# Optimization experiments

Measured on AMD Instinct MI355X. Metric: run time of the kernel, lower is better.

The kernel has to match this reference:

```python
import jax, jax.numpy as jnp
import numpy as np

N = 16384            # number of input vectors
CODEBOOK_SIZE = 8192  # M
DIM = 256             # dim_feature
BETA = 0.25           # commitment_weight


def setup_inputs() -> dict:
    key = jax.random.key(0)
    kx, ke = jax.random.split(key)
    x = jax.random.normal(kx, (N, DIM), dtype=jnp.float32)
    # kaiming-uniform-style init for the codebook
    bound = float(np.sqrt(3.0 / DIM))
    embeddings = jax.random.uniform(ke, (CODEBOOK_SIZE, DIM), dtype=jnp.float32,
                                    minval=-bound, maxval=bound)
    return {"x": x, "embeddings": embeddings}


def reference(x, embeddings):
    # l2_dist: sqrt(sum((x_i - e_j)^2)) computed via the GEMM expansion
    x2 = jnp.sum(x * x, axis=1, keepdims=True)               # (N, 1)
    e2 = jnp.sum(embeddings * embeddings, axis=1)            # (M,)
    d2 = x2 + e2[None, :] - 2.0 * (x @ embeddings.T)         # (N, M)
    dist = jnp.sqrt(jnp.maximum(d2, 0.0))
    # deterministic gumbel_sample path (training eval / stochastic=False):
    # argmax of logits = -dist  <=>  argmin of dist
    ind = jnp.argmin(dist, axis=1)                           # (N,)
    quantized = embeddings[ind]                              # one_hot @ embeddings
    # commitment loss: beta * ||x_q - sg(x)||^2 (docstring)
    commit_loss = BETA * jnp.mean((quantized - jax.lax.stop_gradient(x)) ** 2)
    # straight-through estimator
    quantized_st = x + jax.lax.stop_gradient(quantized - x)
    # perplexity from per-code counts (one-hot scatter)
    counts = jnp.zeros((CODEBOOK_SIZE,), jnp.float32).at[ind].add(1.0)
    probs = counts / counts.sum()
    perplexity = jnp.exp(-jnp.sum(probs * jnp.log(probs + 1e-10)))
    return quantized_st, ind, commit_loss, perplexity
```

## Files before the change

### kernel.cpp

```cpp
#include <hip/hip_runtime.h>
#include <stdint.h>


#define N_VEC 16384
#define M_CODES 8192
#define DIM 256
#define BETA 0.25f

#define NSLICE 4
#define SLICE_CODES 2048
#define BM 256
#define BN 128
#define NPART 8

#define XSLOT 32768
#define ESLOT 16384
#define EBASE (2 * XSLOT)
#define E2OFF (EBASE + 3 * ESLOT)
#define LDS_TOTAL (E2OFF + SLICE_CODES * 4)
#define NSTEPS 128

typedef __attribute__((ext_vector_type(4))) float f32x4;
typedef __attribute__((ext_vector_type(8))) __bf16 bf16x8;

__device__ __forceinline__ void gll16(const void* g, const void* lds_p) {
    __builtin_amdgcn_global_load_lds(
        (const __attribute__((address_space(1))) uint32_t*)(uintptr_t)g,
        (__attribute__((address_space(3))) uint32_t*)(uint32_t)(uintptr_t)lds_p,
        16, 0, 0);
}
#define SB0() __builtin_amdgcn_sched_barrier(0)

__device__ __forceinline__ ushort f2bf(float f) {
    uint32_t u = __float_as_uint(f);
    return (ushort)((u + 0x7FFFu + ((u >> 16) & 1u)) >> 16);
}
__device__ __forceinline__ float bf2f(ushort h) {
    return __uint_as_float(((uint32_t)h) << 16);
}

__global__ __launch_bounds__(256) void prep_kernel(
    const float* __restrict__ x, const float* __restrict__ emb,
    ushort* __restrict__ xh, ushort* __restrict__ xl,
    ushort* __restrict__ eh, ushort* __restrict__ el,
    float* __restrict__ e2, unsigned* __restrict__ counts,
    float* __restrict__ loss_acc) {
    if (blockIdx.x < 8) {
        int4 z = {0, 0, 0, 0};
        ((int4*)counts)[blockIdx.x * 256 + threadIdx.x] = z;
        if (blockIdx.x == 0 && threadIdx.x == 0) *loss_acc = 0.0f;
    }
    const int wave = threadIdx.x >> 6;
    const int lane = threadIdx.x & 63;
    const int row = blockIdx.x * 4 + wave;

    const float* src;
    ushort* ph;
    ushort* pl;
    bool is_e;
    int er = row - N_VEC;
    if (row < N_VEC) {
        src = x + (size_t)row * DIM;
        ph = xh + (size_t)row * DIM;
        pl = xl + (size_t)row * DIM;
        is_e = false;
    } else {
        src = emb + (size_t)er * DIM;
        ph = eh + (size_t)er * DIM;
        pl = el + (size_t)er * DIM;
        is_e = true;
    }
    float4 v = *(const float4*)(src + lane * 4);
    ushort h0 = f2bf(v.x), h1 = f2bf(v.y), h2 = f2bf(v.z), h3 = f2bf(v.w);
    ushort l0 = f2bf(v.x - bf2f(h0)), l1 = f2bf(v.y - bf2f(h1));
    ushort l2 = f2bf(v.z - bf2f(h2)), l3 = f2bf(v.w - bf2f(h3));
    *(ushort4*)(ph + lane * 4) = make_ushort4(h0, h1, h2, h3);
    *(ushort4*)(pl + lane * 4) = make_ushort4(l0, l1, l2, l3);
    if (is_e) {
        float s = v.x * v.x + v.y * v.y + v.z * v.z + v.w * v.w;
        #pragma unroll
        for (int off = 32; off; off >>= 1) s += __shfl_xor(s, off);
        if (lane == 0) e2[er] = s;
    }
}

__global__ __launch_bounds__(512, 1) void vq_mfma_kernel(
    const ushort* __restrict__ xh, const ushort* __restrict__ xl,
    const ushort* __restrict__ eh, const ushort* __restrict__ el,
    const float* __restrict__ e2g, unsigned long long* __restrict__ partials) {
    extern __shared__ char lds[];

    const int t = threadIdx.x;
    const int lane = t & 63;
    const int wv = t >> 6;
    const int lane15 = lane & 15;
    const int l16 = lane >> 4;

    const int rt = blockIdx.x & 63;
    const int slice = blockIdx.x >> 6;
    const int row0 = rt * BM;
    const int cslice0 = slice * SLICE_CODES;

    const int wr0 = (wv & 3) * 64;
    const int wch = wv >> 2;

    const int swz = ((l16 ^ (lane15 >> 1)) & 3) << 4;
    const int byteA0 = (wr0 + lane15) * 64 + swz;
    const int byteB0 = (wch * 64 + lane15) * 64 + swz;

    const int sX0 = wv * 128 + lane;
    const int sX1 = sX0 + 64;
    const int rX0 = sX0 >> 2, rX1 = sX1 >> 2;
    const int cX0 = ((sX0 & 3) ^ ((sX0 >> 3) & 3)) << 3;
    const int cX1 = ((sX1 & 3) ^ ((sX1 >> 3) & 3)) << 3;
    const int sE = wv * 64 + lane;
    const int rE = sE >> 2;
    const int cE = ((sE & 3) ^ ((sE >> 3) & 3)) << 3;

    const ushort* pxh_a = xh + (size_t)(row0 + rX0) * DIM + cX0;
    const ushort* pxh_b = xh + (size_t)(row0 + rX1) * DIM + cX1;
    const ushort* pxl_a = xl + (size_t)(row0 + rX0) * DIM + cX0;
    const ushort* pxl_b = xl + (size_t)(row0 + rX1) * DIM + cX1;
    const ushort* peh = eh + (size_t)(cslice0 + rE) * DIM + cE;
    const ushort* pel = el + (size_t)(cslice0 + rE) * DIM + cE;

    float* e2s = (float*)(lds + E2OFF);
    #pragma unroll
    for (int i = 0; i < 4; ++i) e2s[i * 512 + t] = e2g[cslice0 + i * 512 + t];
    __syncthreads();

    auto stage_X = [&](int s) {
        char* b = lds + (s & 1) * XSLOT + wv * 2048;
        const int xo = (s & 7) * 32;
        gll16(pxh_a + xo, b);
        gll16(pxh_b + xo, b + 1024);
        gll16(pxl_a + xo, b + 16384);
        gll16(pxl_b + xo, b + 16384 + 1024);
    };
    auto stage_E = [&](int slot, int s) {
        char* b = lds + EBASE + slot * ESLOT + wv * 1024;
        const size_t eo = ((size_t)(s >> 3) << 15) + (s & 7) * 32;
        gll16(peh + eo, b);
        gll16(pel + eo, b + 8192);
    };

    float best[16];
    int bidx[16];
    #pragma unroll
    for (int s = 0; s < 16; ++s) { best[s] = __uint_as_float(0x7f800000u); bidx[s] = 0; }

    f32x4 acc[4][4];
    #pragma unroll
    for (int fi = 0; fi < 4; ++fi)
        #pragma unroll
        for (int fj = 0; fj < 4; ++fj) acc[fi][fj] = (f32x4){0.f, 0.f, 0.f, 0.f};

    stage_X(0); SB0();
    stage_E(0, 0); SB0();
    stage_E(1, 1); SB0();

    int esl = 0;
    for (int s = 0; s < NSTEPS; ++s) {
        if (s == NSTEPS - 1) {
            asm volatile("s_waitcnt vmcnt(0)" ::: "memory");
        } else {
            asm volatile("s_waitcnt vmcnt(2)" ::: "memory");
        }
        __builtin_amdgcn_s_barrier();
        SB0();
        if (s + 1 < NSTEPS) { stage_X(s + 1); SB0(); }
        const int stslot = (esl >= 1) ? esl - 1 : 2;
        if (s + 2 < NSTEPS) { stage_E(stslot, s + 2); SB0(); }

        const char* lbX = lds + (s & 1) * XSLOT;
        const char* lbE = lds + EBASE + esl * ESLOT;
        bf16x8 ah[4], alo[4];
        #pragma unroll
        for (int f = 0; f < 4; ++f) {
            ah[f] = *(const bf16x8*)(lbX + byteA0 + f * 1024);
            alo[f] = *(const bf16x8*)(lbX + 16384 + byteA0 + f * 1024);
        }
        __builtin_amdgcn_s_setprio(1);
        #pragma unroll
        for (int fj = 0; fj < 4; ++fj) {
            bf16x8 bh = *(const bf16x8*)(lbE + byteB0 + fj * 1024);
            bf16x8 blo = *(const bf16x8*)(lbE + 8192 + byteB0 + fj * 1024);
            #pragma unroll
            for (int fi = 0; fi < 4; ++fi)
                acc[fi][fj] = __builtin_amdgcn_mfma_f32_16x16x32_bf16(
                    ah[fi], bh, acc[fi][fj], 0, 0, 0);
            #pragma unroll
            for (int fi = 0; fi < 4; ++fi)
                acc[fi][fj] = __builtin_amdgcn_mfma_f32_16x16x32_bf16(
                    ah[fi], blo, acc[fi][fj], 0, 0, 0);
            #pragma unroll
            for (int fi = 0; fi < 4; ++fi)
                acc[fi][fj] = __builtin_amdgcn_mfma_f32_16x16x32_bf16(
                    alo[fi], bh, acc[fi][fj], 0, 0, 0);
        }
        __builtin_amdgcn_s_setprio(0);
        esl = (esl == 2) ? 0 : esl + 1;

        if ((s & 7) == 7) {
            const int ct = s >> 3;
            const int cl = ct * BN + wch * 64 + lane15;
            #pragma unroll
            for (int fj = 0; fj < 4; ++fj) {
                const float e2v = e2s[cl + fj * 16];
                const int c = cslice0 + cl + fj * 16;
                #pragma unroll
                for (int fi = 0; fi < 4; ++fi)
                    #pragma unroll
                    for (int r = 0; r < 4; ++r) {
                        float sc = e2v - 2.0f * acc[fi][fj][r];
                        const int slot = fi * 4 + r;
                        if (sc < best[slot]) { best[slot] = sc; bidx[slot] = c; }
                    }
            }
            #pragma unroll
            for (int fi = 0; fi < 4; ++fi)
                #pragma unroll
                for (int fj = 0; fj < 4; ++fj)
                    acc[fi][fj] = (f32x4){0.f, 0.f, 0.f, 0.f};
        }
    }

    #pragma unroll
    for (int slot = 0; slot < 16; ++slot) {
        float v = best[slot];
        int ix = bidx[slot];
        #pragma unroll
        for (int off = 1; off < 16; off <<= 1) {
            float v2 = __shfl_xor(v, off);
            int ix2 = __shfl_xor(ix, off);
            if (v2 < v || (v2 == v && ix2 < ix)) { v = v2; ix = ix2; }
        }
        if (lane15 == 0) {
            int fi = slot >> 2, r = slot & 3;
            int row = row0 + wr0 + fi * 16 + l16 * 4 + r;
            uint32_t u = __float_as_uint(v);
            uint32_t ord = (u & 0x80000000u) ? ~u : (u | 0x80000000u);
            partials[(size_t)(slice * 2 + wch) * N_VEC + row] =
                ((unsigned long long)ord << 32) | (unsigned)ix;
        }
    }
}

__global__ __launch_bounds__(256) void finish_kernel(
    const float* __restrict__ x, const float* __restrict__ emb,
    const unsigned long long* __restrict__ partials,
    float* __restrict__ out_ind, float* __restrict__ out_q,
    unsigned* __restrict__ counts, float* __restrict__ loss_acc) {
    __shared__ float partial[4];
    const int wave = threadIdx.x >> 6;
    const int lane = threadIdx.x & 63;
    const int row = blockIdx.x * 4 + wave;

    unsigned long long m = ~0ull;
    if (lane < NPART) m = partials[(size_t)lane * N_VEC + row];
    #pragma unroll
    for (int off = 1; off < NPART; off <<= 1) {
        unsigned long long v = __shfl_xor(m, off);
        if (v < m) m = v;
    }
    m = __shfl(m, 0);
    const int ix = (int)(unsigned)(m & 0xFFFFFFFFull);

    float4 q = *(const float4*)(emb + (size_t)ix * DIM + lane * 4);
    float4 xv = *(const float4*)(x + (size_t)row * DIM + lane * 4);
    *(float4*)(out_q + (size_t)row * DIM + lane * 4) = q;
    float dx = q.x - xv.x, dy = q.y - xv.y, dz = q.z - xv.z, dw = q.w - xv.w;
    float s = dx * dx + dy * dy + dz * dz + dw * dw;
    #pragma unroll
    for (int off = 32; off; off >>= 1) s += __shfl_xor(s, off);
    if (lane == 0) {
        out_ind[row] = (float)ix;
        atomicAdd(&counts[ix], 1u);
        partial[wave] = s;
    }
    __syncthreads();
    if (threadIdx.x == 0)
        atomicAdd(loss_acc, partial[0] + partial[1] + partial[2] + partial[3]);
}

__global__ __launch_bounds__(256) void finalize_kernel(
    const unsigned* __restrict__ counts, const float* __restrict__ loss_acc,
    float* __restrict__ out_scalars) {
    __shared__ float red[256];
    float h = 0.0f;
    for (int c = threadIdx.x; c < M_CODES; c += 256) {
        float p = (float)counts[c] * (1.0f / (float)N_VEC);
        h += p * logf(p + 1e-10f);
    }
    red[threadIdx.x] = h;
    __syncthreads();
    for (int s = 128; s; s >>= 1) {
        if (threadIdx.x < s) red[threadIdx.x] += red[threadIdx.x + s];
        __syncthreads();
    }
    if (threadIdx.x == 0) {
        out_scalars[0] = BETA * loss_acc[0] / (float)(N_VEC * DIM);
        out_scalars[1] = expf(-red[0]);
    }
}

extern "C" void kernel_launch(void* const* d_in, const int* in_sizes, int n_in,
                              void* d_out, int out_size, void* d_ws, size_t ws_size,
                              hipStream_t stream) {
    const float* x = (const float*)d_in[0];
    const float* emb = (const float*)d_in[1];

    float* out = (float*)d_out;
    float* out_q = out;
    float* out_ind = out + (size_t)N_VEC * DIM;
    float* out_scalars = out_ind + N_VEC;

    ushort* xh = (ushort*)out;
    ushort* xl = xh + (size_t)N_VEC * DIM;

    char* wp = (char*)d_ws;
    ushort* eh = (ushort*)wp;  wp += (size_t)M_CODES * DIM * 2;
    ushort* el = (ushort*)wp;  wp += (size_t)M_CODES * DIM * 2;
    float* e2 = (float*)wp;    wp += (size_t)M_CODES * 4;
    unsigned long long* partials = (unsigned long long*)wp;
    wp += (size_t)NPART * N_VEC * 8;
    unsigned* counts = (unsigned*)wp; wp += (size_t)M_CODES * 4;
    float* loss_acc = (float*)wp;

    prep_kernel<<<(N_VEC + M_CODES) / 4, 256, 0, stream>>>(x, emb, xh, xl, eh, el,
                                                           e2, counts, loss_acc);

    hipFuncSetAttribute((const void*)vq_mfma_kernel,
                        hipFuncAttributeMaxDynamicSharedMemorySize, LDS_TOTAL);
    vq_mfma_kernel<<<(N_VEC / BM) * NSLICE, 512, LDS_TOTAL, stream>>>(
        xh, xl, eh, el, e2, partials);

    finish_kernel<<<N_VEC / 4, 256, 0, stream>>>(x, emb, partials, out_ind, out_q,
                                                 counts, loss_acc);
    finalize_kernel<<<1, 256, 0, stream>>>(counts, loss_acc, out_scalars);
}
```

Baseline: 262.0 us.

## Triple-buffer X tiles and double-buffer register fragments across MFMA steps

Expands the X LDS staging from two to three slots, matching E, so both X and E for step s+2 load while step s computes. It also adds register double buffering: the LDS fragments for the next step are read into a second register set before the current step's MFMAs run, and the loop is unrolled by two to alternate the sets. The aim is to hide LDS read latency and global-load latency behind the MFMA work. The cost is more LDS (an extra 32KB), doubled fragment registers that can lower occupancy, and a full vmcnt(0)/lgkmcnt(0) wait at every step.

After: 605.9 us. 2.31x slower.

```diff
diff --git a/kernel.cpp b/kernel.cpp
--- a/kernel.cpp
+++ b/kernel.cpp
@@ -15,7 +15,7 @@
 
 #define XSLOT 32768
 #define ESLOT 16384
-#define EBASE (2 * XSLOT)
+#define EBASE (3 * XSLOT)
 #define E2OFF (EBASE + 3 * ESLOT)
 #define LDS_TOTAL (E2OFF + SLICE_CODES * 4)
 #define NSTEPS 128
@@ -129,21 +129,78 @@
     for (int i = 0; i < 4; ++i) e2s[i * 512 + t] = e2g[cslice0 + i * 512 + t];
     __syncthreads();
 
-    auto stage_X = [&](int s) {
-        char* b = lds + (s & 1) * XSLOT + wv * 2048;
+    auto stage_X = [&](int slotOff, int s) {
+        char* b = lds + slotOff + wv * 2048;
         const int xo = (s & 7) * 32;
         gll16(pxh_a + xo, b);
         gll16(pxh_b + xo, b + 1024);
         gll16(pxl_a + xo, b + 16384);
         gll16(pxl_b + xo, b + 16384 + 1024);
     };
-    auto stage_E = [&](int slot, int s) {
-        char* b = lds + EBASE + slot * ESLOT + wv * 1024;
+    auto stage_E = [&](int slotOff, int s) {
+        char* b = lds + slotOff + wv * 1024;
         const size_t eo = ((size_t)(s >> 3) << 15) + (s & 7) * 32;
         gll16(peh + eo, b);
         gll16(pel + eo, b + 8192);
     };
 
+#define PREFETCH(XO, EO, AH, AL, BH, BL) do {                          \
+    const char* lA_ = lds + (XO);                                      \
+    const char* lB_ = lds + (EO);                                      \
+    _Pragma("unroll") for (int f_ = 0; f_ < 4; ++f_) {                 \
+        AH[f_] = *(const bf16x8*)(lA_ + byteA0 + f_ * 1024);           \
+        AL[f_] = *(const bf16x8*)(lA_ + 16384 + byteA0 + f_ * 1024);   \
+        BH[f_] = *(const bf16x8*)(lB_ + byteB0 + f_ * 1024);           \
+        BL[f_] = *(const bf16x8*)(lB_ + 8192 + byteB0 + f_ * 1024);    \
+    } } while (0)
+
+#define MFMA3(AH, AL, BH, BL) do {                                               \
+    _Pragma("unroll") for (int fi_ = 0; fi_ < 4; ++fi_)                          \
+    _Pragma("unroll") for (int fj_ = 0; fj_ < 4; ++fj_)                          \
+        acc[fi_][fj_] = __builtin_amdgcn_mfma_f32_16x16x32_bf16(                 \
+            AH[fi_], BH[fj_], acc[fi_][fj_], 0, 0, 0);                           \
+    _Pragma("unroll") for (int fi_ = 0; fi_ < 4; ++fi_)                          \
+    _Pragma("unroll") for (int fj_ = 0; fj_ < 4; ++fj_)                          \
+        acc[fi_][fj_] = __builtin_amdgcn_mfma_f32_16x16x32_bf16(                 \
+            AH[fi_], BL[fj_], acc[fi_][fj_], 0, 0, 0);                           \
+    _Pragma("unroll") for (int fi_ = 0; fi_ < 4; ++fi_)                          \
+    _Pragma("unroll") for (int fj_ = 0; fj_ < 4; ++fj_)                          \
+        acc[fi_][fj_] = __builtin_amdgcn_mfma_f32_16x16x32_bf16(                 \
+            AL[fi_], BH[fj_], acc[fi_][fj_], 0, 0, 0);                           \
+    } while (0)
+
+#define EPILOGUE(CT) do {                                                        \
+    const int clb_ = (CT) * BN + wch * 64 + lane15;                              \
+    _Pragma("unroll") for (int fj_ = 0; fj_ < 4; ++fj_) {                        \
+        const float e2v_ = e2s[clb_ + fj_ * 16];                                 \
+        const int c_ = cslice0 + clb_ + fj_ * 16;                                \
+        _Pragma("unroll") for (int fi_ = 0; fi_ < 4; ++fi_)                      \
+        _Pragma("unroll") for (int r_ = 0; r_ < 4; ++r_) {                       \
+            float sc_ = e2v_ - 2.0f * acc[fi_][fj_][r_];                         \
+            const int sl_ = fi_ * 4 + r_;                                        \
+            if (sc_ < best[sl_]) { best[sl_] = sc_; bidx[sl_] = c_; }            \
+        }                                                                        \
+    }                                                                            \
+    _Pragma("unroll") for (int fi_ = 0; fi_ < 4; ++fi_)                          \
+    _Pragma("unroll") for (int fj_ = 0; fj_ < 4; ++fj_)                          \
+        acc[fi_][fj_] = (f32x4){0.f, 0.f, 0.f, 0.f};                             \
+    } while (0)
+
+#define STEP(SVAL, CAH, CAL, CBH, CBL, NAH, NAL, NBH, NBL) do {                  \
+    const int s_ = (SVAL);                                                       \
+    asm volatile("s_waitcnt vmcnt(0) lgkmcnt(0)" ::: "memory");                  \
+    SB0();                                                                       \
+    __builtin_amdgcn_s_barrier();                                                \
+    if (s_ + 2 < NSTEPS) { stage_X(xs2, s_ + 2); stage_E(es2, s_ + 2); SB0(); }  \
+    if (s_ + 1 < NSTEPS) { PREFETCH(xs1, es1, NAH, NAL, NBH, NBL); }             \
+    __builtin_amdgcn_s_setprio(1);                                               \
+    MFMA3(CAH, CAL, CBH, CBL);                                                   \
+    __builtin_amdgcn_s_setprio(0);                                               \
+    if ((s_ & 7) == 7) { EPILOGUE(s_ >> 3); }                                    \
+    int tx_ = xs0; xs0 = xs1; xs1 = xs2; xs2 = tx_;                              \
+    int te_ = es0; es0 = es1; es1 = es2; es2 = te_;                              \
+    } while (0)
+
     float best[16];
     int bidx[16];
     #pragma unroll
@@ -155,74 +212,21 @@
         #pragma unroll
         for (int fj = 0; fj < 4; ++fj) acc[fi][fj] = (f32x4){0.f, 0.f, 0.f, 0.f};
 
-    stage_X(0); SB0();
-    stage_E(0, 0); SB0();
-    stage_E(1, 1); SB0();
-
-    int esl = 0;
-    for (int s = 0; s < NSTEPS; ++s) {
-        if (s == NSTEPS - 1) {
-            asm volatile("s_waitcnt vmcnt(0)" ::: "memory");
-        } else {
-            asm volatile("s_waitcnt vmcnt(2)" ::: "memory");
-        }
-        __builtin_amdgcn_s_barrier();
-        SB0();
-        if (s + 1 < NSTEPS) { stage_X(s + 1); SB0(); }
-        const int stslot = (esl >= 1) ? esl - 1 : 2;
-        if (s + 2 < NSTEPS) { stage_E(stslot, s + 2); SB0(); }
-
-        const char* lbX = lds + (s & 1) * XSLOT;
-        const char* lbE = lds + EBASE + esl * ESLOT;
-        bf16x8 ah[4], alo[4];
-        #pragma unroll
-        for (int f = 0; f < 4; ++f) {
-            ah[f] = *(const bf16x8*)(lbX + byteA0 + f * 1024);
-            alo[f] = *(const bf16x8*)(lbX + 16384 + byteA0 + f * 1024);
-        }
-        __builtin_amdgcn_s_setprio(1);
-        #pragma unroll
-        for (int fj = 0; fj < 4; ++fj) {
-            bf16x8 bh = *(const bf16x8*)(lbE + byteB0 + fj * 1024);
-            bf16x8 blo = *(const bf16x8*)(lbE + 8192 + byteB0 + fj * 1024);
-            #pragma unroll
-            for (int fi = 0; fi < 4; ++fi)
-                acc[fi][fj] = __builtin_amdgcn_mfma_f32_16x16x32_bf16(
-                    ah[fi], bh, acc[fi][fj], 0, 0, 0);
-            #pragma unroll
-            for (int fi = 0; fi < 4; ++fi)
-                acc[fi][fj] = __builtin_amdgcn_mfma_f32_16x16x32_bf16(
-                    ah[fi], blo, acc[fi][fj], 0, 0, 0);
-            #pragma unroll
-            for (int fi = 0; fi < 4; ++fi)
-                acc[fi][fj] = __builtin_amdgcn_mfma_f32_16x16x32_bf16(
-                    alo[fi], bh, acc[fi][fj], 0, 0, 0);
-        }
-        __builtin_amdgcn_s_setprio(0);
-        esl = (esl == 2) ? 0 : esl + 1;
-
-        if ((s & 7) == 7) {
-            const int ct = s >> 3;
-            const int cl = ct * BN + wch * 64 + lane15;
-            #pragma unroll
-            for (int fj = 0; fj < 4; ++fj) {
-                const float e2v = e2s[cl + fj * 16];
-                const int c = cslice0 + cl + fj * 16;
-                #pragma unroll
-                for (int fi = 0; fi < 4; ++fi)
-                    #pragma unroll
-                    for (int r = 0; r < 4; ++r) {
-                        float sc = e2v - 2.0f * acc[fi][fj][r];
-                        const int slot = fi * 4 + r;
-                        if (sc < best[slot]) { best[slot] = sc; bidx[slot] = c; }
-                    }
-            }
-            #pragma unroll
-            for (int fi = 0; fi < 4; ++fi)
-                #pragma unroll
-                for (int fj = 0; fj < 4; ++fj)
-                    acc[fi][fj] = (f32x4){0.f, 0.f, 0.f, 0.f};
-        }
+    bf16x8 aH0[4], aL0[4], bH0[4], bL0[4];
+    bf16x8 aH1[4], aL1[4], bH1[4], bL1[4];
+
+    int xs0 = 0, xs1 = XSLOT, xs2 = 2 * XSLOT;
+    int es0 = EBASE, es1 = EBASE + ESLOT, es2 = EBASE + 2 * ESLOT;
+
+    stage_X(xs0, 0); stage_E(es0, 0); SB0();
+    stage_X(xs1, 1); stage_E(es1, 1); SB0();
+    asm volatile("s_waitcnt vmcnt(6)" ::: "memory");
+    __builtin_amdgcn_s_barrier();
+    PREFETCH(xs0, es0, aH0, aL0, bH0, bL0);
+
+    for (int s2 = 0; s2 < NSTEPS / 2; ++s2) {
+        STEP(2 * s2,     aH0, aL0, bH0, bL0, aH1, aL1, bH1, bL1);
+        STEP(2 * s2 + 1, aH1, aL1, bH1, bL1, aH0, aL0, bH0, bL0);
     }
 
     #pragma unroll
```
